# Kernel tuning notes

Hardware: AMD Instinct MI355X
Metric: run time of the kernel (lower is better)

## Reference

```python
import jax, jax.numpy as jnp
import numpy as np

B, D, T = 8, 1024, 512
HID, NH, NL = 256, 4, 2
OUT = HID // NH  # 64 per-head dim
ALPHA = 0.2      # leaky relu slope
EPS = 1e-5       # layernorm eps


def setup_inputs() -> dict:
    key = jax.random.key(0)
    ks = jax.random.split(key, 10)
    X_obs = jax.random.normal(ks[0], (B, D, T), dtype=jnp.float32)
    mask = (jax.random.uniform(ks[1], (B, D, T)) < 0.8).astype(jnp.float32)
    W_in = jax.random.normal(ks[2], (2 * T, HID), dtype=jnp.float32) * (1.0 / np.sqrt(2 * T))
    b_in = jnp.zeros((HID,), dtype=jnp.float32)
    gat_W = jax.random.normal(ks[3], (NL, NH, HID, OUT), dtype=jnp.float32) * (1.0 / np.sqrt(HID))
    gat_a = jax.random.normal(ks[4], (NL, NH, 2 * OUT), dtype=jnp.float32) * 0.1
    ln_g = jnp.ones((NL, HID), dtype=jnp.float32)
    ln_b = jnp.zeros((NL, HID), dtype=jnp.float32)
    W_out = jax.random.normal(ks[5], (HID, T), dtype=jnp.float32) * (1.0 / np.sqrt(HID))
    b_out = jnp.zeros((T,), dtype=jnp.float32)
    return dict(X_obs=X_obs, mask=mask, W_in=W_in, b_in=b_in, gat_W=gat_W,
                gat_a=gat_a, ln_g=ln_g, ln_b=ln_b, W_out=W_out, b_out=b_out)


def _layer_norm(x, g, b):
    mu = jnp.mean(x, axis=-1, keepdims=True)
    var = jnp.mean((x - mu) ** 2, axis=-1, keepdims=True)
    return (x - mu) * jax.lax.rsqrt(var + EPS) * g + b


def _gat_forward(X_obs, mask, W_in, b_in, gat_W, gat_a, ln_g, ln_b, W_out, b_out):
    # mean-impute per (d, t) position across batch
    obs_sum = jnp.sum(X_obs * mask, axis=0, keepdims=True)
    obs_cnt = jnp.sum(mask, axis=0, keepdims=True)
    pos_mean = obs_sum / (obs_cnt + 1e-10)
    X_mean = X_obs * mask + (1.0 - mask) * pos_mean

    x = jnp.concatenate([X_mean, mask], axis=-1)       # (B, D, 2T)
    h = x @ W_in + b_in                                 # (B, N, HID)

    for l in range(NL):
        Wl = gat_W[l]                                   # (H, HID, OUT)
        a_left = gat_a[l, :, :OUT]                      # (H, OUT)
        a_right = gat_a[l, :, OUT:]                     # (H, OUT)
        hW = jnp.einsum('bnd,hde->bhne', h, Wl)         # (B, H, N, OUT)
        # e_ij = leakyrelu(a_left . h_i + a_right . h_j) -- avoids O(N^2 * 2d) concat
        s_l = jnp.einsum('bhne,he->bhn', hW, a_left)
        s_r = jnp.einsum('bhne,he->bhn', hW, a_right)
        e = jax.nn.leaky_relu(s_l[..., :, None] + s_r[..., None, :], ALPHA)  # (B,H,N,N)
        attn = jax.nn.softmax(e, axis=-1)
        head_out = jnp.einsum('bhnm,bhme->bhne', attn, hW)                   # (B,H,N,OUT)
        h_new = jnp.transpose(head_out, (0, 2, 1, 3)).reshape(h.shape[0], h.shape[1], HID)
        h = _layer_norm(h + h_new, ln_g[l], ln_b[l])

    return h @ W_out + b_out                            # (B, D, T)


def reference(X_obs, mask, W_in, b_in, gat_W, gat_a, ln_g, ln_b, W_out, b_out):
    return _gat_forward(X_obs, mask, W_in, b_in, gat_W, gat_a, ln_g, ln_b, W_out, b_out)
```

## Files before the change

kernel.cpp:

```cpp
#include <hip/hip_runtime.h>
#include <hip/hip_bf16.h>

constexpr int B_   = 8;
constexpr int D_   = 1024;
constexpr int T_   = 512;
constexpr int HID_ = 256;
constexpr int NH_  = 4;
constexpr int NL_  = 2;
constexpr int OUT_ = 64;
constexpr float ALPHA_ = 0.2f;
constexpr float EPS_   = 1e-5f;
constexpr int M_ = B_ * D_;
constexpr int DT_ = D_ * T_;
constexpr int KIN_ = 2 * T_;

typedef __attribute__((ext_vector_type(8))) short short8;
typedef __attribute__((ext_vector_type(4))) float floatx4;

__device__ __forceinline__ unsigned short f2bf(float f) {
    unsigned int u = __float_as_uint(f);
    unsigned int r = u + 0x7fffu + ((u >> 16) & 1u);
    return (unsigned short)(r >> 16);
}
__device__ __forceinline__ float bf2f(unsigned short u) {
    return __uint_as_float((unsigned int)u << 16);
}

__global__ __launch_bounds__(256) void impute_k(const float* __restrict__ X,
                                                const float* __restrict__ Mk,
                                                unsigned short* __restrict__ Ain) {
    int idx = blockIdx.x * 256 + threadIdx.x;
    int t = idx & (T_ - 1);
    int d = idx >> 9;
    float x[B_], m[B_];
    float s = 0.f, c = 0.f;
#pragma unroll
    for (int b = 0; b < B_; b++) {
        x[b] = X[(size_t)b * DT_ + idx];
        m[b] = Mk[(size_t)b * DT_ + idx];
        s += x[b] * m[b];
        c += m[b];
    }
    float pm = s / (c + 1e-10f);
#pragma unroll
    for (int b = 0; b < B_; b++) {
        float xm = x[b] * m[b] + (1.f - m[b]) * pm;
        size_t row = (size_t)b * D_ + d;
        Ain[row * KIN_ + t]      = f2bf(xm);
        Ain[row * KIN_ + T_ + t] = f2bf(m[b]);
    }
}

__global__ __launch_bounds__(256) void tconv_k(const float* __restrict__ src,
                                               unsigned short* __restrict__ dst,
                                               int K, int N) {
    int idx = blockIdx.x * 256 + threadIdx.x;
    if (idx >= K * N) return;
    int n = idx / K, k = idx - n * K;
    dst[idx] = f2bf(src[(size_t)k * N + n]);
}

__global__ __launch_bounds__(256) void wcat_t_k(const float* __restrict__ gatW,
                                                unsigned short* __restrict__ Wt) {
    int idx = blockIdx.x * 256 + threadIdx.x;
    int l = idx >> 16;
    int n = (idx >> 8) & 255;
    int k = idx & 255;
    int h = n >> 6, e = n & 63;
    Wt[idx] = f2bf(gatW[(((size_t)(l * NH_ + h) * HID_) + k) * OUT_ + e]);
}

template <int MODE>
__global__ __launch_bounds__(256) void gemm_bf16_k(
        const unsigned short* __restrict__ A,
        const unsigned short* __restrict__ Bt,
        const float* __restrict__ bias,
        float* __restrict__ C,
        unsigned short* __restrict__ Cb,
        int Msz, int Nsz, int Ksz) {
    __shared__ __align__(16) unsigned short As[128 * 32];
    __shared__ __align__(16) unsigned short Bs[64 * 32];
    int tid = threadIdx.x;
    int wave = tid >> 6, lane = tid & 63;
    int q = lane >> 4, r16 = lane & 15;
    int rowbase = blockIdx.y * 128;
    int colbase = blockIdx.x * 64;

    floatx4 acc[2][4];
#pragma unroll
    for (int i = 0; i < 2; i++)
#pragma unroll
        for (int j = 0; j < 4; j++) acc[i][j] = (floatx4)0.f;

    for (int kt = 0; kt < Ksz; kt += 32) {
#pragma unroll
        for (int i = 0; i < 2; i++) {
            int c = tid + i * 256;
            int row = c >> 2, off = (c & 3) * 8;
            *(uint4*)&As[c * 8] =
                *(const uint4*)&A[(size_t)(rowbase + row) * Ksz + kt + off];
        }
        {
            int n = tid >> 2, off = (tid & 3) * 8;
            *(uint4*)&Bs[tid * 8] =
                *(const uint4*)&Bt[(size_t)(colbase + n) * Ksz + kt + off];
        }
        __syncthreads();
        short8 a[2], b[4];
#pragma unroll
        for (int mi = 0; mi < 2; mi++)
            a[mi] = *(const short8*)&As[(wave * 32 + mi * 16 + r16) * 32 + q * 8];
#pragma unroll
        for (int ni = 0; ni < 4; ni++)
            b[ni] = *(const short8*)&Bs[(ni * 16 + r16) * 32 + q * 8];
#pragma unroll
        for (int mi = 0; mi < 2; mi++)
#pragma unroll
            for (int ni = 0; ni < 4; ni++)
                acc[mi][ni] = __builtin_amdgcn_mfma_f32_16x16x32_bf16(
                    a[mi], b[ni], acc[mi][ni], 0, 0, 0);
        __syncthreads();
    }
    if constexpr (MODE == 2) {
        int bhh = ((rowbase >> 10) << 2) + blockIdx.x;
        int mbase = (rowbase & (D_ - 1)) + wave * 32;
#pragma unroll
        for (int mi = 0; mi < 2; mi++) {
#pragma unroll
            for (int ni = 0; ni < 4; ni++) {
                int e = ni * 16 + r16;
                ushort4 pk;
                pk.x = f2bf(acc[mi][ni][0]);
                pk.y = f2bf(acc[mi][ni][1]);
                pk.z = f2bf(acc[mi][ni][2]);
                pk.w = f2bf(acc[mi][ni][3]);
                int mloc = mbase + mi * 16 + q * 4;
                *(ushort4*)&Cb[((size_t)(bhh * 64 + e) << 10) + mloc] = pk;
            }
        }
    } else {
#pragma unroll
        for (int mi = 0; mi < 2; mi++) {
#pragma unroll
            for (int rr = 0; rr < 4; rr++) {
                int row = rowbase + wave * 32 + mi * 16 + q * 4 + rr;
#pragma unroll
                for (int ni = 0; ni < 4; ni++) {
                    int col = colbase + ni * 16 + r16;
                    float v = acc[mi][ni][rr] + (bias ? bias[col] : 0.f);
                    C[(size_t)row * Nsz + col] = v;
                    if constexpr (MODE == 1) Cb[(size_t)row * Nsz + col] = f2bf(v);
                }
            }
        }
    }
}

__global__ __launch_bounds__(256) void slr_k(const unsigned short* __restrict__ hwT,
                                             const float* __restrict__ gat_a,
                                             int l,
                                             float* __restrict__ s_l,
                                             float* __restrict__ s_r,
                                             float* __restrict__ rmax4) {
    int bh = blockIdx.x;
    int h = bh & 3;
    int n = blockIdx.y * 256 + threadIdx.x;
    __shared__ float al[OUT_], ar[OUT_];
    __shared__ float red[256];
    if (threadIdx.x < OUT_)
        al[threadIdx.x] = gat_a[(size_t)(l * NH_ + h) * 2 * OUT_ + threadIdx.x];
    else if (threadIdx.x < 2 * OUT_)
        ar[threadIdx.x - OUT_] = gat_a[(size_t)(l * NH_ + h) * 2 * OUT_ + threadIdx.x];
    __syncthreads();
    const unsigned short* base = hwT + ((size_t)(bh * 64) << 10) + n;
    float sl = 0.f, sr = 0.f;
#pragma unroll 8
    for (int e = 0; e < OUT_; e++) {
        float v = bf2f(base[(size_t)e << 10]);
        sl += v * al[e];
        sr += v * ar[e];
    }
    s_l[bh * D_ + n] = sl;
    s_r[bh * D_ + n] = sr;
    red[threadIdx.x] = sr;
    __syncthreads();
    for (int s = 128; s > 0; s >>= 1) {
        if (threadIdx.x < s) red[threadIdx.x] = fmaxf(red[threadIdx.x], red[threadIdx.x + s]);
        __syncthreads();
    }
    if (threadIdx.x == 0) rmax4[bh * 4 + blockIdx.y] = red[0];
}

__global__ __launch_bounds__(256) void attn_k(const unsigned short* __restrict__ hwT,
                                              const float* __restrict__ sl_g,
                                              const float* __restrict__ sr_g,
                                              const float* __restrict__ rmax4,
                                              float* __restrict__ hnew) {
    int bh = blockIdx.x;
    int b = bh >> 2, h = bh & 3;
    int tid = threadIdx.x;
    int wave = tid >> 6, lane = tid & 63;
    int q = lane >> 4, r16 = lane & 15;

    __shared__ float srs[D_];
    __shared__ __align__(16) unsigned short Vt[64][136];
    __shared__ float den_lds[64];

    *(float4*)&srs[tid * 4] = *(const float4*)&sr_g[bh * D_ + tid * 4];

    float rm = fmaxf(fmaxf(rmax4[bh * 4 + 0], rmax4[bh * 4 + 1]),
                     fmaxf(rmax4[bh * 4 + 2], rmax4[bh * 4 + 3]));
    int row0 = blockIdx.y * 64 + wave * 16;
    float sl = sl_g[bh * D_ + row0 + r16];
    float xm = sl + rm;
    float Mn = fmaxf(xm, ALPHA_ * xm);

    floatx4 acc[4];
#pragma unroll
    for (int i = 0; i < 4; i++) acc[i] = (floatx4)0.f;
    float dsum = 0.f;

    const unsigned short* vbase = hwT + ((size_t)(bh * 64) << 10);

    for (int mc = 0; mc < D_; mc += 128) {
        __syncthreads();
#pragma unroll
        for (int i = 0; i < 4; i++) {
            int s = tid + i * 256;
            int e = s >> 4, part = s & 15;
            *(uint4*)&Vt[e][part * 8] = *(const uint4*)&vbase[((size_t)e << 10) + mc + part * 8];
        }
        __syncthreads();
#pragma unroll
        for (int kk = 0; kk < 128; kk += 32) {
            int m0 = mc + kk + q * 8;
            float4 s0 = *(const float4*)&srs[m0];
            float4 s1 = *(const float4*)&srs[m0 + 4];
            float sr8[8] = {s0.x, s0.y, s0.z, s0.w, s1.x, s1.y, s1.z, s1.w};
            float p[8];
#pragma unroll
            for (int j = 0; j < 8; j++) {
                float x = sl + sr8[j];
                float e = fmaxf(x, ALPHA_ * x);
                float pj = __expf(e - Mn);
                dsum += pj;
                p[j] = pj;
            }
            union { unsigned int u[4]; short8 s8; } cv;
#pragma unroll
            for (int j = 0; j < 4; j++) {
                unsigned int lo = (__float_as_uint(p[2 * j]) + 0x8000u) >> 16;
                unsigned int hi = (__float_as_uint(p[2 * j + 1]) + 0x8000u) & 0xffff0000u;
                cv.u[j] = hi | lo;
            }
#pragma unroll
            for (int ni = 0; ni < 4; ni++) {
                short8 bfr = *(const short8*)&Vt[ni * 16 + r16][kk + q * 8];
                acc[ni] = __builtin_amdgcn_mfma_f32_16x16x32_bf16(cv.s8, bfr, acc[ni], 0, 0, 0);
            }
        }
    }
    dsum += __shfl_xor(dsum, 16);
    dsum += __shfl_xor(dsum, 32);
    if (q == 0) den_lds[wave * 16 + r16] = dsum;
    __syncthreads();
#pragma unroll
    for (int rr = 0; rr < 4; rr++) {
        int rloc = q * 4 + rr;
        float rden = 1.f / den_lds[wave * 16 + rloc];
        size_t grow = (size_t)(b * D_ + blockIdx.y * 64 + wave * 16 + rloc);
#pragma unroll
        for (int ni = 0; ni < 4; ni++) {
            hnew[grow * HID_ + h * OUT_ + ni * 16 + r16] = acc[ni][rr] * rden;
        }
    }
}

__global__ __launch_bounds__(256) void addln_k(float* __restrict__ h,
                                               const float* __restrict__ hn,
                                               const float* __restrict__ g,
                                               const float* __restrict__ bb,
                                               unsigned short* __restrict__ hbf) {
    int row = blockIdx.x;
    int c = threadIdx.x;
    float v = h[(size_t)row * HID_ + c] + hn[(size_t)row * HID_ + c];
    __shared__ float red[256];
    red[c] = v;
    __syncthreads();
    for (int s = 128; s > 0; s >>= 1) {
        if (c < s) red[c] += red[c + s];
        __syncthreads();
    }
    float mu = red[0] * (1.f / HID_);
    __syncthreads();
    float d = v - mu;
    red[c] = d * d;
    __syncthreads();
    for (int s = 128; s > 0; s >>= 1) {
        if (c < s) red[c] += red[c + s];
        __syncthreads();
    }
    float var = red[0] * (1.f / HID_);
    float res = d * rsqrtf(var + EPS_) * g[c] + bb[c];
    h[(size_t)row * HID_ + c]   = res;
    hbf[(size_t)row * HID_ + c] = f2bf(res);
}

extern "C" void kernel_launch(void* const* d_in, const int* in_sizes, int n_in,
                              void* d_out, int out_size, void* d_ws, size_t ws_size,
                              hipStream_t stream) {
    const float* X_obs = (const float*)d_in[0];
    const float* mask  = (const float*)d_in[1];
    const float* W_in  = (const float*)d_in[2];
    const float* b_in  = (const float*)d_in[3];
    const float* gat_W = (const float*)d_in[4];
    const float* gat_a = (const float*)d_in[5];
    const float* ln_g  = (const float*)d_in[6];
    const float* ln_b  = (const float*)d_in[7];
    const float* W_out = (const float*)d_in[8];
    const float* b_out = (const float*)d_in[9];
    float* out = (float*)d_out;

    char* base = (char*)d_ws;
    unsigned short* Ain  = (unsigned short*)base;
    unsigned short* hwT  = (unsigned short*)base;
    float* hnew = (float*)(base + (4u << 20));
    float* hbuf = (float*)(base + (16u << 20));
    unsigned short* hbf   = (unsigned short*)(base + (24u << 20));
    unsigned short* Wt_in = (unsigned short*)(base + (28u << 20));
    unsigned short* Wcat  = Wt_in + (size_t)HID_ * KIN_;
    unsigned short* WtO   = Wcat + (size_t)NL_ * HID_ * HID_;
    float* slb = (float*)(WtO + (size_t)T_ * HID_);
    float* srb = slb + B_ * NH_ * D_;
    float* rmx = srb + B_ * NH_ * D_;

    impute_k<<<DT_ / 256, 256, 0, stream>>>(X_obs, mask, Ain);
    tconv_k<<<(KIN_ * HID_) / 256, 256, 0, stream>>>(W_in, Wt_in, KIN_, HID_);
    wcat_t_k<<<(NL_ * HID_ * HID_) / 256, 256, 0, stream>>>(gat_W, Wcat);
    tconv_k<<<(HID_ * T_) / 256, 256, 0, stream>>>(W_out, WtO, HID_, T_);

    gemm_bf16_k<1><<<dim3(HID_ / 64, M_ / 128), 256, 0, stream>>>(
        Ain, Wt_in, b_in, hbuf, hbf, M_, HID_, KIN_);

    for (int l = 0; l < NL_; l++) {
        gemm_bf16_k<2><<<dim3(HID_ / 64, M_ / 128), 256, 0, stream>>>(
            hbf, Wcat + (size_t)l * HID_ * HID_, nullptr, nullptr, hwT, M_, HID_, HID_);
        slr_k<<<dim3(B_ * NH_, 4), 256, 0, stream>>>(hwT, gat_a, l, slb, srb, rmx);
        attn_k<<<dim3(B_ * NH_, D_ / 64), 256, 0, stream>>>(hwT, slb, srb, rmx, hnew);
        addln_k<<<M_, 256, 0, stream>>>(hbuf, hnew, ln_g + (size_t)l * HID_,
                                        ln_b + (size_t)l * HID_, hbf);
    }

    gemm_bf16_k<0><<<dim3(T_ / 64, M_ / 128), 256, 0, stream>>>(
        hbf, WtO, b_out, out, nullptr, M_, T_, HID_);
}
```

Before: 238.0 us.

## Fuse attention-score projection into GEMM epilogue, double-buffer GEMM, vectorize prep and layernorm

Folds the s_l/s_r projection and the per-(b,h) row max into the MODE-2 GEMM epilogue, using wave shuffles and an atomicMax on order-preserving encoded floats. This removes the separate slr_k kernel and its re-read of hwT. The GEMM now double-buffers its LDS tiles with register prefetch, so each k-step needs only one barrier. The three weight-transpose kernels merge into one launch that also clears the max keys. The impute and add+layernorm kernels are vectorized to float4, with layernorm reduced per wave through shuffles instead of shared-memory tree reductions. The costs are extra atomics and epilogue register pressure in the GEMM.

```diff
diff --git a/kernel.cpp b/kernel.cpp
--- a/kernel.cpp
+++ b/kernel.cpp
@@ -25,49 +25,71 @@
 __device__ __forceinline__ float bf2f(unsigned short u) {
     return __uint_as_float((unsigned int)u << 16);
 }
+__device__ __forceinline__ unsigned int kenc(float f) {
+    unsigned int u = __float_as_uint(f);
+    return (u & 0x80000000u) ? ~u : (u | 0x80000000u);
+}
+__device__ __forceinline__ float kdec(unsigned int k) {
+    unsigned int u = (k & 0x80000000u) ? (k ^ 0x80000000u) : ~k;
+    return __uint_as_float(u);
+}
 
 __global__ __launch_bounds__(256) void impute_k(const float* __restrict__ X,
                                                 const float* __restrict__ Mk,
                                                 unsigned short* __restrict__ Ain) {
+    int idx4 = (blockIdx.x * 256 + threadIdx.x) * 4;
+    int t = idx4 & (T_ - 1);
+    int d = idx4 >> 9;
+    float4 x[B_], m[B_];
+    float4 s = {0, 0, 0, 0}, c = {0, 0, 0, 0};
+#pragma unroll
+    for (int b = 0; b < B_; b++) {
+        x[b] = *(const float4*)&X[(size_t)b * DT_ + idx4];
+        m[b] = *(const float4*)&Mk[(size_t)b * DT_ + idx4];
+        s.x += x[b].x * m[b].x; s.y += x[b].y * m[b].y;
+        s.z += x[b].z * m[b].z; s.w += x[b].w * m[b].w;
+        c.x += m[b].x; c.y += m[b].y; c.z += m[b].z; c.w += m[b].w;
+    }
+    float4 pm;
+    pm.x = s.x / (c.x + 1e-10f); pm.y = s.y / (c.y + 1e-10f);
+    pm.z = s.z / (c.z + 1e-10f); pm.w = s.w / (c.w + 1e-10f);
+#pragma unroll
+    for (int b = 0; b < B_; b++) {
+        size_t row = (size_t)b * D_ + d;
+        ushort4 xm, mk;
+        xm.x = f2bf(x[b].x * m[b].x + (1.f - m[b].x) * pm.x);
+        xm.y = f2bf(x[b].y * m[b].y + (1.f - m[b].y) * pm.y);
+        xm.z = f2bf(x[b].z * m[b].z + (1.f - m[b].z) * pm.z);
+        xm.w = f2bf(x[b].w * m[b].w + (1.f - m[b].w) * pm.w);
+        mk.x = f2bf(m[b].x); mk.y = f2bf(m[b].y);
+        mk.z = f2bf(m[b].z); mk.w = f2bf(m[b].w);
+        *(ushort4*)&Ain[row * KIN_ + t]      = xm;
+        *(ushort4*)&Ain[row * KIN_ + T_ + t] = mk;
+    }
+}
+
+__global__ __launch_bounds__(256) void wprep_k(const float* __restrict__ W_in,
+                                               const float* __restrict__ gatW,
+                                               const float* __restrict__ W_out,
+                                               unsigned short* __restrict__ Wt_in,
+                                               unsigned short* __restrict__ Wcat,
+                                               unsigned short* __restrict__ WtO,
+                                               unsigned int* __restrict__ rmaxkey) {
     int idx = blockIdx.x * 256 + threadIdx.x;
-    int t = idx & (T_ - 1);
-    int d = idx >> 9;
-    float x[B_], m[B_];
-    float s = 0.f, c = 0.f;
-#pragma unroll
-    for (int b = 0; b < B_; b++) {
-        x[b] = X[(size_t)b * DT_ + idx];
-        m[b] = Mk[(size_t)b * DT_ + idx];
-        s += x[b] * m[b];
-        c += m[b];
-    }
-    float pm = s / (c + 1e-10f);
-#pragma unroll
-    for (int b = 0; b < B_; b++) {
-        float xm = x[b] * m[b] + (1.f - m[b]) * pm;
-        size_t row = (size_t)b * D_ + d;
-        Ain[row * KIN_ + t]      = f2bf(xm);
-        Ain[row * KIN_ + T_ + t] = f2bf(m[b]);
-    }
-}
-
-__global__ __launch_bounds__(256) void tconv_k(const float* __restrict__ src,
-                                               unsigned short* __restrict__ dst,
-                                               int K, int N) {
-    int idx = blockIdx.x * 256 + threadIdx.x;
-    if (idx >= K * N) return;
-    int n = idx / K, k = idx - n * K;
-    dst[idx] = f2bf(src[(size_t)k * N + n]);
-}
-
-__global__ __launch_bounds__(256) void wcat_t_k(const float* __restrict__ gatW,
-                                                unsigned short* __restrict__ Wt) {
-    int idx = blockIdx.x * 256 + threadIdx.x;
-    int l = idx >> 16;
-    int n = (idx >> 8) & 255;
-    int k = idx & 255;
-    int h = n >> 6, e = n & 63;
-    Wt[idx] = f2bf(gatW[(((size_t)(l * NH_ + h) * HID_) + k) * OUT_ + e]);
+    if (idx < 64) rmaxkey[idx] = 0u;
+    if (idx < 262144) {
+        int n = idx >> 10, k = idx & 1023;
+        Wt_in[idx] = f2bf(W_in[(size_t)k * HID_ + n]);
+    } else if (idx < 393216) {
+        int j = idx - 262144;
+        int l = j >> 16, n = (j >> 8) & 255, k = j & 255;
+        int h = n >> 6, e = n & 63;
+        Wcat[j] = f2bf(gatW[(((size_t)(l * NH_ + h) * HID_) + k) * OUT_ + e]);
+    } else {
+        int j = idx - 393216;
+        int n = j >> 8, k = j & 255;
+        WtO[j] = f2bf(W_out[(size_t)k * T_ + n]);
+    }
 }
 
 template <int MODE>
@@ -77,53 +99,72 @@
         const float* __restrict__ bias,
         float* __restrict__ C,
         unsigned short* __restrict__ Cb,
-        int Msz, int Nsz, int Ksz) {
-    __shared__ __align__(16) unsigned short As[128 * 32];
-    __shared__ __align__(16) unsigned short Bs[64 * 32];
+        const float* __restrict__ ga,
+        float* __restrict__ s_l,
+        float* __restrict__ s_r,
+        unsigned int* __restrict__ rmaxkey,
+        int Nsz, int Ksz) {
+    __shared__ __align__(16) unsigned short As[2][128 * 32];
+    __shared__ __align__(16) unsigned short Bs[2][64 * 32];
     int tid = threadIdx.x;
     int wave = tid >> 6, lane = tid & 63;
     int q = lane >> 4, r16 = lane & 15;
     int rowbase = blockIdx.y * 128;
     int colbase = blockIdx.x * 64;
 
+    int arow0 = tid >> 2,        aoff0 = (tid & 3) * 8;
+    int arow1 = (tid + 256) >> 2, aoff1 = (tid & 3) * 8;
+    int brow = tid >> 2, boff = (tid & 3) * 8;
+    const unsigned short* Ap0 = A + (size_t)(rowbase + arow0) * Ksz + aoff0;
+    const unsigned short* Ap1 = A + (size_t)(rowbase + arow1) * Ksz + aoff1;
+    const unsigned short* Bp  = Bt + (size_t)(colbase + brow) * Ksz + boff;
+
     floatx4 acc[2][4];
 #pragma unroll
     for (int i = 0; i < 2; i++)
 #pragma unroll
         for (int j = 0; j < 4; j++) acc[i][j] = (floatx4)0.f;
 
-    for (int kt = 0; kt < Ksz; kt += 32) {
-#pragma unroll
-        for (int i = 0; i < 2; i++) {
-            int c = tid + i * 256;
-            int row = c >> 2, off = (c & 3) * 8;
-            *(uint4*)&As[c * 8] =
-                *(const uint4*)&A[(size_t)(rowbase + row) * Ksz + kt + off];
-        }
-        {
-            int n = tid >> 2, off = (tid & 3) * 8;
-            *(uint4*)&Bs[tid * 8] =
-                *(const uint4*)&Bt[(size_t)(colbase + n) * Ksz + kt + off];
-        }
+    uint4 ar0 = *(const uint4*)Ap0;
+    uint4 ar1 = *(const uint4*)Ap1;
+    uint4 br  = *(const uint4*)Bp;
+    *(uint4*)&As[0][tid * 8]         = ar0;
+    *(uint4*)&As[0][(tid + 256) * 8] = ar1;
+    *(uint4*)&Bs[0][tid * 8]         = br;
+
+    int nk = Ksz >> 5;
+    for (int it = 0; it < nk; it++) {
+        int cur = it & 1;
         __syncthreads();
+        if (it + 1 < nk) {
+            int kt2 = (it + 1) << 5;
+            ar0 = *(const uint4*)(Ap0 + kt2);
+            ar1 = *(const uint4*)(Ap1 + kt2);
+            br  = *(const uint4*)(Bp + kt2);
+        }
         short8 a[2], b[4];
 #pragma unroll
         for (int mi = 0; mi < 2; mi++)
-            a[mi] = *(const short8*)&As[(wave * 32 + mi * 16 + r16) * 32 + q * 8];
+            a[mi] = *(const short8*)&As[cur][(wave * 32 + mi * 16 + r16) * 32 + q * 8];
 #pragma unroll
         for (int ni = 0; ni < 4; ni++)
-            b[ni] = *(const short8*)&Bs[(ni * 16 + r16) * 32 + q * 8];
+            b[ni] = *(const short8*)&Bs[cur][(ni * 16 + r16) * 32 + q * 8];
 #pragma unroll
         for (int mi = 0; mi < 2; mi++)
 #pragma unroll
             for (int ni = 0; ni < 4; ni++)
                 acc[mi][ni] = __builtin_amdgcn_mfma_f32_16x16x32_bf16(
                     a[mi], b[ni], acc[mi][ni], 0, 0, 0);
-        __syncthreads();
+        if (it + 1 < nk) {
+            int nxt = cur ^ 1;
+            *(uint4*)&As[nxt][tid * 8]         = ar0;
+            *(uint4*)&As[nxt][(tid + 256) * 8] = ar1;
+            *(uint4*)&Bs[nxt][tid * 8]         = br;
+        }
     }
     if constexpr (MODE == 2) {
         int bhh = ((rowbase >> 10) << 2) + blockIdx.x;
-        int mbase = (rowbase & (D_ - 1)) + wave * 32;
+        int nbase = (rowbase & (D_ - 1)) + wave * 32;
 #pragma unroll
         for (int mi = 0; mi < 2; mi++) {
 #pragma unroll
@@ -134,10 +175,53 @@
                 pk.y = f2bf(acc[mi][ni][1]);
                 pk.z = f2bf(acc[mi][ni][2]);
                 pk.w = f2bf(acc[mi][ni][3]);
-                int mloc = mbase + mi * 16 + q * 4;
-                *(ushort4*)&Cb[((size_t)(bhh * 64 + e) << 10) + mloc] = pk;
-            }
-        }
+                *(ushort4*)&Cb[((size_t)(bhh * 64 + e) << 10) + nbase + mi * 16 + q * 4] = pk;
+            }
+        }
+        const float* gab = ga + blockIdx.x * 2 * OUT_;
+        float al4[4], ar4[4];
+#pragma unroll
+        for (int ni = 0; ni < 4; ni++) {
+            al4[ni] = gab[ni * 16 + r16];
+            ar4[ni] = gab[OUT_ + ni * 16 + r16];
+        }
+        float slv[2][4], srv[2][4];
+#pragma unroll
+        for (int mi = 0; mi < 2; mi++)
+#pragma unroll
+            for (int rr = 0; rr < 4; rr++) {
+                float s1 = 0.f, s2 = 0.f;
+#pragma unroll
+                for (int ni = 0; ni < 4; ni++) {
+                    s1 += acc[mi][ni][rr] * al4[ni];
+                    s2 += acc[mi][ni][rr] * ar4[ni];
+                }
+                slv[mi][rr] = s1;
+                srv[mi][rr] = s2;
+            }
+#pragma unroll
+        for (int off = 1; off < 16; off <<= 1) {
+#pragma unroll
+            for (int mi = 0; mi < 2; mi++)
+#pragma unroll
+                for (int rr = 0; rr < 4; rr++) {
+                    slv[mi][rr] += __shfl_xor(slv[mi][rr], off, 64);
+                    srv[mi][rr] += __shfl_xor(srv[mi][rr], off, 64);
+                }
+        }
+        {
+            int slot = r16 & 7;
+            int mi = slot >> 2, rr = slot & 3;
+            int n = nbase + mi * 16 + q * 4 + rr;
+            if (r16 < 8) s_l[bhh * D_ + n] = slv[mi][rr];
+            else         s_r[bhh * D_ + n] = srv[mi][rr];
+        }
+        float mx = -1e30f;
+#pragma unroll
+        for (int mi = 0; mi < 2; mi++)
+#pragma unroll
+            for (int rr = 0; rr < 4; rr++) mx = fmaxf(mx, srv[mi][rr]);
+        if (lane == 0) atomicMax(&rmaxkey[bhh], kenc(mx));
     } else {
 #pragma unroll
         for (int mi = 0; mi < 2; mi++) {
@@ -156,45 +240,10 @@
     }
 }
 
-__global__ __launch_bounds__(256) void slr_k(const unsigned short* __restrict__ hwT,
-                                             const float* __restrict__ gat_a,
-                                             int l,
-                                             float* __restrict__ s_l,
-                                             float* __restrict__ s_r,
-                                             float* __restrict__ rmax4) {
-    int bh = blockIdx.x;
-    int h = bh & 3;
-    int n = blockIdx.y * 256 + threadIdx.x;
-    __shared__ float al[OUT_], ar[OUT_];
-    __shared__ float red[256];
-    if (threadIdx.x < OUT_)
-        al[threadIdx.x] = gat_a[(size_t)(l * NH_ + h) * 2 * OUT_ + threadIdx.x];
-    else if (threadIdx.x < 2 * OUT_)
-        ar[threadIdx.x - OUT_] = gat_a[(size_t)(l * NH_ + h) * 2 * OUT_ + threadIdx.x];
-    __syncthreads();
-    const unsigned short* base = hwT + ((size_t)(bh * 64) << 10) + n;
-    float sl = 0.f, sr = 0.f;
-#pragma unroll 8
-    for (int e = 0; e < OUT_; e++) {
-        float v = bf2f(base[(size_t)e << 10]);
-        sl += v * al[e];
-        sr += v * ar[e];
-    }
-    s_l[bh * D_ + n] = sl;
-    s_r[bh * D_ + n] = sr;
-    red[threadIdx.x] = sr;
-    __syncthreads();
-    for (int s = 128; s > 0; s >>= 1) {
-        if (threadIdx.x < s) red[threadIdx.x] = fmaxf(red[threadIdx.x], red[threadIdx.x + s]);
-        __syncthreads();
-    }
-    if (threadIdx.x == 0) rmax4[bh * 4 + blockIdx.y] = red[0];
-}
-
 __global__ __launch_bounds__(256) void attn_k(const unsigned short* __restrict__ hwT,
                                               const float* __restrict__ sl_g,
                                               const float* __restrict__ sr_g,
-                                              const float* __restrict__ rmax4,
+                                              const unsigned int* __restrict__ rmaxkey,
                                               float* __restrict__ hnew) {
     int bh = blockIdx.x;
     int b = bh >> 2, h = bh & 3;
@@ -208,8 +257,7 @@
 
     *(float4*)&srs[tid * 4] = *(const float4*)&sr_g[bh * D_ + tid * 4];
 
-    float rm = fmaxf(fmaxf(rmax4[bh * 4 + 0], rmax4[bh * 4 + 1]),
-                     fmaxf(rmax4[bh * 4 + 2], rmax4[bh * 4 + 3]));
+    float rm = kdec(rmaxkey[bh]);
     int row0 = blockIdx.y * 64 + wave * 16;
     float sl = sl_g[bh * D_ + row0 + r16];
     float xm = sl + rm;
@@ -281,29 +329,30 @@
                                                const float* __restrict__ g,
                                                const float* __restrict__ bb,
                                                unsigned short* __restrict__ hbf) {
-    int row = blockIdx.x;
-    int c = threadIdx.x;
-    float v = h[(size_t)row * HID_ + c] + hn[(size_t)row * HID_ + c];
-    __shared__ float red[256];
-    red[c] = v;
-    __syncthreads();
-    for (int s = 128; s > 0; s >>= 1) {
-        if (c < s) red[c] += red[c + s];
-        __syncthreads();
-    }
-    float mu = red[0] * (1.f / HID_);
-    __syncthreads();
-    float d = v - mu;
-    red[c] = d * d;
-    __syncthreads();
-    for (int s = 128; s > 0; s >>= 1) {
-        if (c < s) red[c] += red[c + s];
-        __syncthreads();
-    }
-    float var = red[0] * (1.f / HID_);
-    float res = d * rsqrtf(var + EPS_) * g[c] + bb[c];
-    h[(size_t)row * HID_ + c]   = res;
-    hbf[(size_t)row * HID_ + c] = f2bf(res);
+    int wave = threadIdx.x >> 6, lane = threadIdx.x & 63;
+    size_t row = (size_t)blockIdx.x * 4 + wave;
+    float4 a = *(const float4*)&h[row * HID_ + lane * 4];
+    float4 r = *(const float4*)&hn[row * HID_ + lane * 4];
+    float4 v = {a.x + r.x, a.y + r.y, a.z + r.z, a.w + r.w};
+    float s = v.x + v.y + v.z + v.w;
+#pragma unroll
+    for (int off = 1; off < 64; off <<= 1) s += __shfl_xor(s, off, 64);
+    float mu = s * (1.f / HID_);
+    float4 d = {v.x - mu, v.y - mu, v.z - mu, v.w - mu};
+    float s2 = d.x * d.x + d.y * d.y + d.z * d.z + d.w * d.w;
+#pragma unroll
+    for (int off = 1; off < 64; off <<= 1) s2 += __shfl_xor(s2, off, 64);
+    float rs = rsqrtf(s2 * (1.f / HID_) + EPS_);
+    float4 gg = *(const float4*)&g[lane * 4];
+    float4 bbv = *(const float4*)&bb[lane * 4];
+    float4 res;
+    res.x = d.x * rs * gg.x + bbv.x;
+    res.y = d.y * rs * gg.y + bbv.y;
+    res.z = d.z * rs * gg.z + bbv.z;
+    res.w = d.w * rs * gg.w + bbv.w;
+    *(float4*)&h[row * HID_ + lane * 4] = res;
+    ushort4 pk = {f2bf(res.x), f2bf(res.y), f2bf(res.z), f2bf(res.w)};
+    *(ushort4*)&hbf[row * HID_ + lane * 4] = pk;
 }
 
 extern "C" void kernel_launch(void* const* d_in, const int* in_sizes, int n_in,
@@ -332,25 +381,27 @@
     unsigned short* WtO   = Wcat + (size_t)NL_ * HID_ * HID_;
     float* slb = (float*)(WtO + (size_t)T_ * HID_);
     float* srb = slb + B_ * NH_ * D_;
-    float* rmx = srb + B_ * NH_ * D_;
-
-    impute_k<<<DT_ / 256, 256, 0, stream>>>(X_obs, mask, Ain);
-    tconv_k<<<(KIN_ * HID_) / 256, 256, 0, stream>>>(W_in, Wt_in, KIN_, HID_);
-    wcat_t_k<<<(NL_ * HID_ * HID_) / 256, 256, 0, stream>>>(gat_W, Wcat);
-    tconv_k<<<(HID_ * T_) / 256, 256, 0, stream>>>(W_out, WtO, HID_, T_);
+    unsigned int* rmaxkey = (unsigned int*)(srb + B_ * NH_ * D_);
+
+    impute_k<<<DT_ / 1024, 256, 0, stream>>>(X_obs, mask, Ain);
+    wprep_k<<<2048, 256, 0, stream>>>(W_in, gat_W, W_out, Wt_in, Wcat, WtO, rmaxkey);
 
     gemm_bf16_k<1><<<dim3(HID_ / 64, M_ / 128), 256, 0, stream>>>(
-        Ain, Wt_in, b_in, hbuf, hbf, M_, HID_, KIN_);
+        Ain, Wt_in, b_in, hbuf, hbf, nullptr, nullptr, nullptr, nullptr,
+        HID_, KIN_);
 
     for (int l = 0; l < NL_; l++) {
         gemm_bf16_k<2><<<dim3(HID_ / 64, M_ / 128), 256, 0, stream>>>(
-            hbf, Wcat + (size_t)l * HID_ * HID_, nullptr, nullptr, hwT, M_, HID_, HID_);
-        slr_k<<<dim3(B_ * NH_, 4), 256, 0, stream>>>(hwT, gat_a, l, slb, srb, rmx);
-        attn_k<<<dim3(B_ * NH_, D_ / 64), 256, 0, stream>>>(hwT, slb, srb, rmx, hnew);
-        addln_k<<<M_, 256, 0, stream>>>(hbuf, hnew, ln_g + (size_t)l * HID_,
-                                        ln_b + (size_t)l * HID_, hbf);
+            hbf, Wcat + (size_t)l * HID_ * HID_, nullptr, nullptr, hwT,
+            gat_a + (size_t)l * NH_ * 2 * OUT_, slb, srb, rmaxkey + l * 32,
+            HID_, HID_);
+        attn_k<<<dim3(B_ * NH_, D_ / 64), 256, 0, stream>>>(
+            hwT, slb, srb, rmaxkey + l * 32, hnew);
+        addln_k<<<M_ / 4, 256, 0, stream>>>(hbuf, hnew, ln_g + (size_t)l * HID_,
+                                            ln_b + (size_t)l * HID_, hbf);
     }
 
     gemm_bf16_k<0><<<dim3(T_ / 64, M_ / 128), 256, 0, stream>>>(
-        hbf, WtO, b_out, out, nullptr, M_, T_, HID_);
-}
+        hbf, WtO, b_out, out, nullptr, nullptr, nullptr, nullptr, nullptr,
+        T_, HID_);
+}
```

Measured after the change: 223.3 us. 1.07x faster.
